# Kernel tuning notes

Hardware: AMD Instinct MI355X
Metric: run time of the kernel (lower is better)

## Reference

```python
import jax, jax.numpy as jnp
import numpy as np
from jax import lax


def _lstm_dir(x, W_ih, W_hh, b, reverse):
    # x: [B, T, D]; torch gate order i, f, g, o
    B, T, D = x.shape
    Hh = W_hh.shape[1]
    h0 = jnp.zeros((B, Hh), x.dtype)
    c0 = jnp.zeros((B, Hh), x.dtype)

    def step(carry, xt):
        h, c = carry
        g = xt @ W_ih.T + h @ W_hh.T + b
        i, f, gg, o = jnp.split(g, 4, axis=-1)
        c = jax.nn.sigmoid(f) * c + jax.nn.sigmoid(i) * jnp.tanh(gg)
        h = jax.nn.sigmoid(o) * jnp.tanh(c)
        return (h, c), h

    _, hs = lax.scan(step, (h0, c0), jnp.swapaxes(x, 0, 1), reverse=reverse)
    return jnp.swapaxes(hs, 0, 1)  # [B, T, Hh]


def _bilstm(x, w_ih_f, w_hh_f, b_f, w_ih_b, w_hh_b, b_b):
    fwd = _lstm_dir(x, w_ih_f, w_hh_f, b_f, reverse=False)
    bwd = _lstm_dir(x, w_ih_b, w_hh_b, b_b, reverse=True)
    return jnp.concatenate([fwd, bwd], axis=-1)


def setup_inputs() -> dict:
    key = jax.random.key(0)
    B, NS, L, H, LH, C = 8, 32, 128, 768, 256, 4
    ks = jax.random.split(key, 16)
    s = 0.05
    inp = {
        "hidden_states": jax.random.normal(ks[0], (B, NS, L, H), jnp.float32),
        "attention_mask": jax.random.randint(ks[1], (B, NS, L), 0, 2, jnp.int32),
        "wl_ih_f": jax.random.normal(ks[2], (4 * LH, H), jnp.float32) * s,
        "wl_hh_f": jax.random.normal(ks[3], (4 * LH, LH), jnp.float32) * s,
        "wl_b_f": jnp.zeros((4 * LH,), jnp.float32).at[LH:2 * LH].set(1.0),
        "wl_ih_b": jax.random.normal(ks[4], (4 * LH, H), jnp.float32) * s,
        "wl_hh_b": jax.random.normal(ks[5], (4 * LH, LH), jnp.float32) * s,
        "wl_b_b": jnp.zeros((4 * LH,), jnp.float32).at[LH:2 * LH].set(1.0),
        "ws_ih_f": jax.random.normal(ks[6], (4 * LH, 2 * LH), jnp.float32) * s,
        "ws_hh_f": jax.random.normal(ks[7], (4 * LH, LH), jnp.float32) * s,
        "ws_b_f": jnp.zeros((4 * LH,), jnp.float32).at[LH:2 * LH].set(1.0),
        "ws_ih_b": jax.random.normal(ks[8], (4 * LH, 2 * LH), jnp.float32) * s,
        "ws_hh_b": jax.random.normal(ks[9], (4 * LH, LH), jnp.float32) * s,
        "ws_b_b": jnp.zeros((4 * LH,), jnp.float32).at[LH:2 * LH].set(1.0),
        "cls_w": jax.random.uniform(ks[10], (C, 2 * LH), jnp.float32, -0.1, 0.1),
        "cls_b": jax.random.uniform(ks[11], (C,), jnp.float32, -0.1, 0.1),
    }
    return inp


def reference(hidden_states, attention_mask,
              wl_ih_f, wl_hh_f, wl_b_f, wl_ih_b, wl_hh_b, wl_b_b,
              ws_ih_f, ws_hh_f, ws_b_f, ws_ih_b, ws_hh_b, ws_b_b,
              cls_w, cls_b):
    B, NS, L, H = hidden_states.shape
    x = hidden_states.reshape(B * NS, L, H)
    m = attention_mask.reshape(B * NS, L).astype(x.dtype)

    # word-level bidirectional LSTM over each sentence
    h = _bilstm(x, wl_ih_f, wl_hh_f, wl_b_f, wl_ih_b, wl_hh_b, wl_b_b)  # [BN, L, 2LH]

    # per-sentence masked mean pooling (zeros for fully-masked sentences)
    cnt = m.sum(-1, keepdims=True)                    # [BN, 1]
    emb = jnp.einsum('btd,bt->bd', h, m) / jnp.maximum(cnt, 1.0)
    emb = jnp.where(cnt > 0, emb, 0.0)                # [BN, 2LH]
    emb = emb.reshape(B, NS, -1)

    # sentence-level bidirectional LSTM
    s = _bilstm(emb, ws_ih_f, ws_hh_f, ws_b_f, ws_ih_b, ws_hh_b, ws_b_b)  # [B, NS, 2LH]

    final = s[:, -1, :]  # dropout is identity in deterministic reference
    logits = final @ cls_w.T + cls_b
    return logits
```

## Files before the change

kernel.cpp:

```cpp
#include <hip/hip_runtime.h>
#include <math.h>


typedef __bf16 bf16x8 __attribute__((ext_vector_type(8)));
typedef float  f32x4  __attribute__((ext_vector_type(4)));

__device__ __forceinline__ float sigmoidf_(float x){ return 1.0f/(1.0f+expf(-x)); }
__device__ __forceinline__ unsigned short f2bf(float x){
    unsigned int b = __float_as_uint(x);
    b += 0x7FFFu + ((b>>16)&1u);
    return (unsigned short)(b>>16);
}
__device__ __forceinline__ float bf2f(unsigned short h){
    return __uint_as_float(((unsigned int)h)<<16);
}
__device__ __forceinline__ void split_bf(float x, unsigned short &hi, unsigned short &lo){
    hi = f2bf(x);
    lo = f2bf(x - bf2f(hi));
}
__device__ __forceinline__ uint4 pack8(const unsigned short* s){
    uint4 u;
    u.x = (unsigned)s[0] | ((unsigned)s[1]<<16);
    u.y = (unsigned)s[2] | ((unsigned)s[3]<<16);
    u.z = (unsigned)s[4] | ((unsigned)s[5]<<16);
    u.w = (unsigned)s[6] | ((unsigned)s[7]<<16);
    return u;
}

__device__ __forceinline__ void group_barrier(int* p, int members, int tid) {
    __syncthreads();
    if (tid == 0) {
        __hip_atomic_fetch_add(p, 1, __ATOMIC_RELAXED, __HIP_MEMORY_SCOPE_AGENT);
        int it = 0;
        while (__hip_atomic_load(p, __ATOMIC_RELAXED, __HIP_MEMORY_SCOPE_AGENT) < members) {
            __builtin_amdgcn_s_sleep(1);
            if (++it > (1<<22)) break;
        }
    }
    __builtin_amdgcn_fence(__ATOMIC_ACQUIRE, "workgroup");
    __syncthreads();
}

__device__ __forceinline__ unsigned tpat(int bid, int tid, int r) {
    unsigned v = (unsigned)bid * 1315423911u ^ (unsigned)tid * 2654435761u ^ 0x9E3779B9u;
    return r ? ~v : v;
}

__global__ void zero_f4(float4* __restrict__ p, int n) {
    int i = blockIdx.x * 256 + threadIdx.x;
    if (i < n) p[i] = make_float4(0.f, 0.f, 0.f, 0.f);
}

__global__ void prep_x(const float* __restrict__ X, unsigned short* __restrict__ Xsw) {
    int idx = blockIdx.x * 256 + threadIdx.x;
    int gblk = idx >> 6, ln = idx & 63;
    int mt = gblk / 24, kb = gblk - mt * 24;
    int m = mt * 16 + (ln & 15);
    int k = kb * 32 + (ln >> 4) * 8;
    const float* xp = X + (size_t)m * 768 + k;
    unsigned short hi[8], lo[8];
#pragma unroll
    for (int e = 0; e < 8; e += 4) {
        float4 v = *(const float4*)(xp + e);
        split_bf(v.x, hi[e+0], lo[e+0]);
        split_bf(v.y, hi[e+1], lo[e+1]);
        split_bf(v.z, hi[e+2], lo[e+2]);
        split_bf(v.w, hi[e+3], lo[e+3]);
    }
    *(uint4*)&Xsw[(size_t)gblk*1024 + ln*8]       = pack8(hi);
    *(uint4*)&Xsw[(size_t)gblk*1024 + 512 + ln*8] = pack8(lo);
}

__global__ void prep_wih_sw(const float* __restrict__ Wf, const float* __restrict__ Wb,
                            unsigned short* __restrict__ Wsw) {
    int idx = blockIdx.x * 256 + threadIdx.x;
    int gblk = idx >> 6, ln = idx & 63;
    int dir = gblk / 1536;
    int rem = gblk - dir * 1536;
    int ntile = rem / 24, kb = rem - ntile * 24;
    int j = ntile * 16 + (ln & 15);
    int k = kb * 32 + (ln >> 4) * 8;
    const float* wp = (dir ? Wb : Wf) + (size_t)j * 768 + k;
    unsigned short hi[8], lo[8];
#pragma unroll
    for (int e = 0; e < 8; e += 4) {
        float4 v = *(const float4*)(wp + e);
        split_bf(v.x, hi[e+0], lo[e+0]);
        split_bf(v.y, hi[e+1], lo[e+1]);
        split_bf(v.z, hi[e+2], lo[e+2]);
        split_bf(v.w, hi[e+3], lo[e+3]);
    }
    *(uint4*)&Wsw[(size_t)gblk*1024 + ln*8]       = pack8(hi);
    *(uint4*)&Wsw[(size_t)gblk*1024 + 512 + ln*8] = pack8(lo);
}

__global__ void prep_whh(const float* __restrict__ Wf, const float* __restrict__ Wb,
                         unsigned short* __restrict__ Wimg) {
    int idx = blockIdx.x * 256 + threadIdx.x;
    if (idx >= 524288) return;
    int dir = idx >> 18;
    int r   = idx & 262143;
    int u0t = r >> 14;
    int g   = (r >> 12) & 3;
    int u   = (r >> 8) & 15;
    int k   = r & 255;
    const float* W = dir ? Wb : Wf;
    float v = W[(size_t)(g*256 + u0t*16 + u) * 256 + k];
    unsigned short hi, lo; split_bf(v, hi, lo);
    size_t base = (size_t)(dir*16 + u0t) * 34816;
    Wimg[base + (g*16 + u)*264 + k]         = hi;
    Wimg[base + 16896 + (g*16 + u)*264 + k] = lo;
}

__global__ void transpose_whh(const float* __restrict__ Wf, const float* __restrict__ Wb,
                              float* __restrict__ Wt) {
    int idx = blockIdx.x * 256 + threadIdx.x;
    if (idx >= 524288) return;
    int dir = idx >> 18;
    int rem = idx & 262143;
    int k = rem >> 10;
    int j = rem & 1023;
    const float* Wp = dir ? Wb : Wf;
    Wt[idx] = Wp[j * 256 + k];
}

__global__ __launch_bounds__(256, 2) void proj_mfma(
    const unsigned short* __restrict__ Xsw,
    const unsigned short* __restrict__ Wihsw,
    const float* __restrict__ bfw, const float* __restrict__ bbw,
    float* __restrict__ Of, float* __restrict__ Ob)
{
    __shared__ unsigned short lds[24576];
    const int tid = threadIdx.x;
    const int nt = blockIdx.x;
    const int mt = blockIdx.y;
    const int sel = nt >> 3;
    const int ntl = nt & 7;
    const float* bias = sel ? bbw : bfw;
    float* Op = sel ? Ob : Of;
    const int wv = tid >> 6, ln = tid & 63;
    const int c = ln & 15, q = ln >> 4;

    f32x4 acc[4][8];
#pragma unroll
    for (int i = 0; i < 4; i++)
#pragma unroll
        for (int j = 0; j < 8; j++) acc[i][j] = f32x4{0.f,0.f,0.f,0.f};

    const unsigned short* Abase = Xsw + (size_t)(mt*16) * 24 * 1024;
    const unsigned short* Bbase = Wihsw + (size_t)(sel*64 + ntl*8) * 24 * 1024;

#pragma unroll 1
    for (int kb = 0; kb < 24; kb++) {
        __syncthreads();
#pragma unroll
        for (int jj = 0; jj < 12; jj++) {
            int cc = wv + 4*jj;
            int isB = (cc >= 32);
            int blk = isB ? ((cc - 32) >> 1) : (cc >> 1);
            int half = cc & 1;
            const unsigned short* src = (isB ? Bbase : Abase)
                                        + (size_t)(blk*24 + kb)*1024 + half*512 + ln*8;
            unsigned short* dst = lds + (isB ? 16384 : 0) + blk*1024 + half*512 + ln*8;
            __builtin_amdgcn_global_load_lds(
                (const __attribute__((address_space(1))) unsigned int*)src,
                (__attribute__((address_space(3))) unsigned int*)dst, 16, 0, 0);
        }
        __syncthreads();

        bf16x8 bhv[8], blv[8];
#pragma unroll
        for (int cb = 0; cb < 8; cb++) {
            bhv[cb] = *(const bf16x8*)&lds[16384 + cb*1024 + ln*8];
            blv[cb] = *(const bf16x8*)&lds[16384 + cb*1024 + 512 + ln*8];
        }
#pragma unroll
        for (int rb = 0; rb < 4; rb++) {
            int it = wv*4 + rb;
            bf16x8 ah = *(const bf16x8*)&lds[it*1024 + ln*8];
            bf16x8 al = *(const bf16x8*)&lds[it*1024 + 512 + ln*8];
#pragma unroll
            for (int cb = 0; cb < 8; cb++) {
                acc[rb][cb] = __builtin_amdgcn_mfma_f32_16x16x32_bf16(ah, bhv[cb], acc[rb][cb], 0,0,0);
                acc[rb][cb] = __builtin_amdgcn_mfma_f32_16x16x32_bf16(ah, blv[cb], acc[rb][cb], 0,0,0);
                acc[rb][cb] = __builtin_amdgcn_mfma_f32_16x16x32_bf16(al, bhv[cb], acc[rb][cb], 0,0,0);
            }
        }
    }

#pragma unroll
    for (int rb = 0; rb < 4; rb++) {
        int mbase = mt*256 + (wv*4 + rb)*16 + q*4;
#pragma unroll
        for (int cb = 0; cb < 8; cb++) {
            int j = ntl*128 + cb*16 + c;
            float bv = bias[j];
#pragma unroll
            for (int reg = 0; reg < 4; reg++) {
                int m = mbase + reg;
                int tt = m & 127, nn = m >> 7;
                Op[(size_t)(tt*256 + nn)*1024 + j] = acc[rb][cb][reg] + bv;
            }
        }
    }
}

__global__ __launch_bounds__(256, 1) void word_recur(
    const float* __restrict__ Gf, const float* __restrict__ Gb,
    const unsigned short* __restrict__ Wimg,
    unsigned short* __restrict__ hA, unsigned short* __restrict__ hB,
    const int* __restrict__ mask,
    float* __restrict__ pooled, int* __restrict__ cnt,
    int* __restrict__ pf, unsigned int* __restrict__ tstg)
{
    extern __shared__ char ldsbuf[];
    unsigned short* Hl = (unsigned short*)ldsbuf;
    float* gex   = (float*)(ldsbuf + 36864);
    int*   mk_lds= (int*)(ldsbuf + 46080);

    const int tid = threadIdx.x;
    const int bid = blockIdx.x;
    const int dir = (bid >> 3) & 1;
    const int nt  = bid & 7;
    const int u0t = bid >> 4;
    const int grp = bid & 15;
    const float* G = dir ? Gb : Gf;

    const int wv = tid >> 6, ln = tid & 63;
    const int c = ln & 15, q = ln >> 4;

    int* mycnt = cnt + grp * 136;

    bool fast;
    {
        unsigned* tl  = (unsigned*)ldsbuf;
        int* oks = (int*)(ldsbuf + 4096);
        int okl = 1;
#pragma unroll 1
        for (int r = 0; r < 2; r++) {
            __hip_atomic_store(&tstg[bid*256 + tid], tpat(bid, tid, r),
                               __ATOMIC_RELAXED, __HIP_MEMORY_SCOPE_AGENT);
            group_barrier(mycnt + 127 + 2*r, 16, tid);
            {
                int pbid = grp + 16*((u0t + 1 + wv) & 15);
                __builtin_amdgcn_global_load_lds(
                    (const __attribute__((address_space(1))) unsigned int*)
                        ((const char*)(tstg + pbid*256) + ln*16),
                    (__attribute__((address_space(3))) unsigned int*)(ldsbuf + wv*1024),
                    16, 0, 0x11 );
            }
            __syncthreads();
#pragma unroll
            for (int w2 = 0; w2 < 4; w2++) {
                int pb2 = grp + 16*((u0t + 1 + w2) & 15);
                okl &= (tl[w2*256 + tid] == tpat(pb2, tid, r)) ? 1 : 0;
            }
            group_barrier(mycnt + 128 + 2*r, 16, tid);
        }
        oks[tid] = okl;
        __syncthreads();
        if (tid == 0) {
            int o = 1;
            for (int i = 0; i < 256; i++) o &= oks[i];
            __hip_atomic_store(&pf[bid], o, __ATOMIC_RELAXED, __HIP_MEMORY_SCOPE_AGENT);
        }
        group_barrier(mycnt + 131, 16, tid);
        int f = 1;
#pragma unroll 1
        for (int k = 0; k < 16; k++)
            f &= __hip_atomic_load(&pf[grp + 16*k],
                                   __ATOMIC_RELAXED, __HIP_MEMORY_SCOPE_AGENT);
        fast = (f != 0);
    }

    {
        const char* msrc = (const char*)(mask + nt*32*128);
#pragma unroll
        for (int j = 0; j < 4; j++) {
            int i = wv + 4*j;
            __builtin_amdgcn_global_load_lds(
                (const __attribute__((address_space(1))) unsigned int*)(msrc + i*1024 + ln*16),
                (__attribute__((address_space(3))) unsigned int*)(((char*)mk_lds) + i*1024), 16, 0, 0);
        }
    }
    const unsigned short* wbase = Wimg + (size_t)(dir*16 + u0t) * 34816;
    bf16x8 wh_[8], wlo[8];
#pragma unroll
    for (int kb = 0; kb < 8; kb++) {
        wh_[kb] = *(const bf16x8*)&wbase[(wv*16 + c)*264 + kb*32 + q*8];
        wlo[kb] = *(const bf16x8*)&wbase[16896 + (wv*16 + c)*264 + kb*32 + q*8];
    }

    const int nl  = tid >> 3;
    const int up  = tid & 7;
    const int u0  = up*2;
    const int ug0 = u0t*16 + u0;
    const int n   = nt*32 + nl;

    float c0 = 0.f, c1 = 0.f, p0 = 0.f, p1 = 0.f;

    float2 gp[4];
    {
        const int te0 = dir ? 127 : 0;
        const float* Ga = G + (size_t)(te0*256 + n)*1024 + ug0;
#pragma unroll
        for (int g = 0; g < 4; g++) gp[g] = *(const float2*)&Ga[g*256];
    }

#pragma unroll 1
    for (int t = 0; t < 128; ++t) {
        const int te = dir ? (127 - t) : t;
        const unsigned short* hin = (t & 1) ? hB : hA;
        unsigned short* hout = ((t & 1) ? hA : hB) + (size_t)(dir*8 + nt) * 18432;

        if (fast) {
            const char* hsrc = (const char*)(hin + (size_t)(dir*8 + nt) * 18432);
#pragma unroll
            for (int j = 0; j < 9; j++) {
                int i = wv + 4*j;
                __builtin_amdgcn_global_load_lds(
                    (const __attribute__((address_space(1))) unsigned int*)(hsrc + i*1024 + ln*16),
                    (__attribute__((address_space(3))) unsigned int*)(ldsbuf + i*1024),
                    16, 0, 0x11 );
            }
        } else {
            const unsigned long long* hsrc =
                (const unsigned long long*)(hin + (size_t)(dir*8 + nt) * 18432);
            unsigned long long* hdst = (unsigned long long*)ldsbuf;
#pragma unroll
            for (int j = 0; j < 18; j++) {
                unsigned long long v = __hip_atomic_load(hsrc + tid + 256*j,
                        __ATOMIC_RELAXED, __HIP_MEMORY_SCOPE_AGENT);
                hdst[tid + 256*j] = v;
            }
        }
        __syncthreads();

        f32x4 acc[2];
        acc[0] = f32x4{0.f,0.f,0.f,0.f};
        acc[1] = f32x4{0.f,0.f,0.f,0.f};
#pragma unroll
        for (int kb = 0; kb < 8; kb++) {
#pragma unroll
            for (int sb = 0; sb < 2; sb++) {
                bf16x8 bh = *(const bf16x8*)&Hl[(sb*16 + c)*264 + kb*32 + q*8];
                bf16x8 bl = *(const bf16x8*)&Hl[8448 + (sb*16 + c)*264 + kb*32 + q*8];
                acc[sb] = __builtin_amdgcn_mfma_f32_16x16x32_bf16(wh_[kb], bh, acc[sb], 0, 0, 0);
                acc[sb] = __builtin_amdgcn_mfma_f32_16x16x32_bf16(wh_[kb], bl, acc[sb], 0, 0, 0);
                acc[sb] = __builtin_amdgcn_mfma_f32_16x16x32_bf16(wlo[kb], bh, acc[sb], 0, 0, 0);
            }
        }
#pragma unroll
        for (int sb = 0; sb < 2; sb++)
#pragma unroll
            for (int reg = 0; reg < 4; reg++)
                gex[(wv*16 + q*4 + reg)*36 + sb*16 + c] = acc[sb][reg];
        __syncthreads();

        float2 gpn[4];
        if (t < 127) {
            const int te1 = dir ? (126 - t) : (t + 1);
            const float* Ga = G + (size_t)(te1*256 + n)*1024 + ug0;
#pragma unroll
            for (int g = 0; g < 4; g++) gpn[g] = *(const float2*)&Ga[g*256];
        }

        const int mk = mk_lds[nl*128 + te];
        float iv0 = gex[(0*16 + u0)*36 + nl] + gp[0].x;
        float fv0 = gex[(1*16 + u0)*36 + nl] + gp[1].x;
        float gv0 = gex[(2*16 + u0)*36 + nl] + gp[2].x;
        float ov0 = gex[(3*16 + u0)*36 + nl] + gp[3].x;
        float iv1 = gex[(0*16 + u0+1)*36 + nl] + gp[0].y;
        float fv1 = gex[(1*16 + u0+1)*36 + nl] + gp[1].y;
        float gv1 = gex[(2*16 + u0+1)*36 + nl] + gp[2].y;
        float ov1 = gex[(3*16 + u0+1)*36 + nl] + gp[3].y;
        float cn0 = sigmoidf_(fv0)*c0 + sigmoidf_(iv0)*tanhf(gv0);
        float hn0 = sigmoidf_(ov0)*tanhf(cn0);
        float cn1 = sigmoidf_(fv1)*c1 + sigmoidf_(iv1)*tanhf(gv1);
        float hn1 = sigmoidf_(ov1)*tanhf(cn1);
        c0 = cn0; c1 = cn1;
        if (mk) { p0 += hn0; p1 += hn1; }
        if (t != 127) {
            unsigned short h0h, h0l, h1h, h1l;
            split_bf(hn0, h0h, h0l);
            split_bf(hn1, h1h, h1l);
            unsigned int dhi = (unsigned)h0h | ((unsigned)h1h << 16);
            unsigned int dlo = (unsigned)h0l | ((unsigned)h1l << 16);
            unsigned int* hw = (unsigned int*)hout;
            __hip_atomic_store(&hw[nl*132 + u0t*8 + up], dhi,
                               __ATOMIC_RELAXED, __HIP_MEMORY_SCOPE_AGENT);
            __hip_atomic_store(&hw[4224 + nl*132 + u0t*8 + up], dlo,
                               __ATOMIC_RELAXED, __HIP_MEMORY_SCOPE_AGENT);
        }

        if (t < 127) {
            group_barrier(mycnt + t, 16, tid);
#pragma unroll
            for (int g = 0; g < 4; g++) gp[g] = gpn[g];
        }
    }

    *(float2*)&pooled[n*512 + dir*256 + ug0] = make_float2(p0, p1);
}

__global__ __launch_bounds__(256) void word_step_mfma(
    const float* __restrict__ Gf, const float* __restrict__ Gb,
    const unsigned short* __restrict__ Wimg,
    const unsigned short* __restrict__ hin_img,
    unsigned short* __restrict__ hout_img,
    const int* __restrict__ mask,
    float* __restrict__ c_st, float* __restrict__ pooled, int t)
{
    extern __shared__ char ldsbuf[];
    unsigned short* Wl = (unsigned short*)ldsbuf;
    unsigned short* Hl = Wl + 34816;
    float* gex = (float*)(ldsbuf + 69632 + 36864);

    const int tid = threadIdx.x;
    const int bid = blockIdx.x;
    const int dir = bid >> 7;
    const int u0t = (bid >> 3) & 15;
    const int nt  = bid & 7;
    const int te  = dir ? (127 - t) : t;
    const float* G = dir ? Gb : Gf;

    const int wv = tid >> 6, ln = tid & 63;
    const int c = ln & 15, q = ln >> 4;

    {
        const char* wsrc = (const char*)(Wimg + (size_t)(dir*16 + u0t) * 34816);
        const char* hsrc = (const char*)(hin_img + (size_t)(dir*8 + nt) * 18432);
        char* wdst = (char*)Wl;
        char* hdst = (char*)Hl;
#pragma unroll
        for (int j = 0; j < 17; j++) {
            int i = wv + 4*j;
            __builtin_amdgcn_global_load_lds(
                (const __attribute__((address_space(1))) unsigned int*)(wsrc + i*1024 + ln*16),
                (__attribute__((address_space(3))) unsigned int*)(wdst + i*1024), 16, 0, 0);
        }
#pragma unroll
        for (int j = 0; j < 9; j++) {
            int i = wv + 4*j;
            __builtin_amdgcn_global_load_lds(
                (const __attribute__((address_space(1))) unsigned int*)(hsrc + i*1024 + ln*16),
                (__attribute__((address_space(3))) unsigned int*)(hdst + i*1024), 16, 0, 0);
        }
    }

    const int uu = tid & 15;
    const int np = tid >> 4;
    const int uglob = u0t*16 + uu;
    const int n_a = nt*32 + np*2;
    float gpre[8]; int mk0, mk1; float cold0, cold1, pold0, pold1;
    {
        const float* Ga = G + (size_t)(te*256 + n_a)*1024 + uglob;
        const float* Gc = Ga + 1024;
#pragma unroll
        for (int g = 0; g < 4; g++) { gpre[g] = Ga[g*256]; gpre[4+g] = Gc[g*256]; }
        mk0 = mask[n_a*128 + te];
        mk1 = mask[(n_a + 1)*128 + te];
        cold0 = c_st[dir*65536 + n_a*256 + uglob];
        cold1 = c_st[dir*65536 + (n_a + 1)*256 + uglob];
        pold0 = pooled[n_a*512 + dir*256 + uglob];
        pold1 = pooled[(n_a + 1)*512 + dir*256 + uglob];
    }
    __syncthreads();

    f32x4 acc[2];
    acc[0] = f32x4{0.f,0.f,0.f,0.f};
    acc[1] = f32x4{0.f,0.f,0.f,0.f};
#pragma unroll
    for (int kb = 0; kb < 8; kb++) {
        bf16x8 ahh = *(const bf16x8*)&Wl[(wv*16 + c)*264 + kb*32 + q*8];
        bf16x8 all_ = *(const bf16x8*)&Wl[16896 + (wv*16 + c)*264 + kb*32 + q*8];
#pragma unroll
        for (int sb = 0; sb < 2; sb++) {
            bf16x8 bh = *(const bf16x8*)&Hl[(sb*16 + c)*264 + kb*32 + q*8];
            bf16x8 bl = *(const bf16x8*)&Hl[8448 + (sb*16 + c)*264 + kb*32 + q*8];
            acc[sb] = __builtin_amdgcn_mfma_f32_16x16x32_bf16(ahh, bh, acc[sb], 0, 0, 0);
            acc[sb] = __builtin_amdgcn_mfma_f32_16x16x32_bf16(ahh, bl, acc[sb], 0, 0, 0);
            acc[sb] = __builtin_amdgcn_mfma_f32_16x16x32_bf16(all_, bh, acc[sb], 0, 0, 0);
        }
    }
#pragma unroll
    for (int sb = 0; sb < 2; sb++)
#pragma unroll
        for (int reg = 0; reg < 4; reg++)
            gex[(wv*16 + q*4 + reg)*36 + sb*16 + c] = acc[sb][reg];
    __syncthreads();

    unsigned short* hout = hout_img + (size_t)(dir*8 + nt) * 18432;
    {
        int nl = np*2;
        float iv = gex[(0*16 + uu)*36 + nl] + gpre[0];
        float fv = gex[(1*16 + uu)*36 + nl] + gpre[1];
        float gv = gex[(2*16 + uu)*36 + nl] + gpre[2];
        float ov = gex[(3*16 + uu)*36 + nl] + gpre[3];
        float cn = sigmoidf_(fv)*cold0 + sigmoidf_(iv)*tanhf(gv);
        float hn = sigmoidf_(ov)*tanhf(cn);
        c_st[dir*65536 + n_a*256 + uglob] = cn;
        unsigned short hh, hl; split_bf(hn, hh, hl);
        hout[nl*264 + uglob] = hh;
        hout[8448 + nl*264 + uglob] = hl;
        if (mk0) pooled[n_a*512 + dir*256 + uglob] = pold0 + hn;
    }
    {
        int nl = np*2 + 1;
        float iv = gex[(0*16 + uu)*36 + nl] + gpre[4];
        float fv = gex[(1*16 + uu)*36 + nl] + gpre[5];
        float gv = gex[(2*16 + uu)*36 + nl] + gpre[6];
        float ov = gex[(3*16 + uu)*36 + nl] + gpre[7];
        float cn = sigmoidf_(fv)*cold1 + sigmoidf_(iv)*tanhf(gv);
        float hn = sigmoidf_(ov)*tanhf(cn);
        c_st[dir*65536 + (n_a+1)*256 + uglob] = cn;
        unsigned short hh, hl; split_bf(hn, hh, hl);
        hout[nl*264 + uglob] = hh;
        hout[8448 + nl*264 + uglob] = hl;
        if (mk1) pooled[(n_a+1)*512 + dir*256 + uglob] = pold1 + hn;
    }
}

__global__ __launch_bounds__(256) void gemm_proj(
    const float* __restrict__ A, int M, int K,
    const float* __restrict__ Wf, const float* __restrict__ Wb,
    const float* __restrict__ bf, const float* __restrict__ bb,
    float* __restrict__ Of, float* __restrict__ Ob)
{
    __shared__ float As[16][132];
    __shared__ float Bs[16][132];
    const int t = threadIdx.x;
    const int n0 = blockIdx.x * 128;
    const int m0 = blockIdx.y * 128;
    const int sel = (n0 >= 1024);
    const float* Wp = sel ? Wb : Wf;
    const float* bp = sel ? bb : bf;
    float* Op = sel ? Ob : Of;
    const int n0d = n0 & 1023;
    const int tm = t >> 4;
    const int tn = t & 15;

    float acc[8][8];
#pragma unroll
    for (int i = 0; i < 8; i++)
#pragma unroll
        for (int j = 0; j < 8; j++) acc[i][j] = 0.f;

    for (int k0 = 0; k0 < K; k0 += 16) {
        __syncthreads();
#pragma unroll
        for (int rr = 0; rr < 2; rr++) {
            int idx = t + rr * 256;
            int row = idx >> 2, kq = idx & 3;
            float4 v = *(const float4*)&A[(size_t)(m0 + row) * K + k0 + kq * 4];
            As[kq*4+0][row] = v.x; As[kq*4+1][row] = v.y;
            As[kq*4+2][row] = v.z; As[kq*4+3][row] = v.w;
        }
#pragma unroll
        for (int rr = 0; rr < 2; rr++) {
            int idx = t + rr * 256;
            int row = idx >> 2, kq = idx & 3;
            float4 v = *(const float4*)&Wp[(size_t)(n0d + row) * K + k0 + kq * 4];
            Bs[kq*4+0][row] = v.x; Bs[kq*4+1][row] = v.y;
            Bs[kq*4+2][row] = v.z; Bs[kq*4+3][row] = v.w;
        }
        __syncthreads();
#pragma unroll
        for (int k = 0; k < 16; k++) {
            float4 a0 = *(const float4*)&As[k][tm*4];
            float4 a1 = *(const float4*)&As[k][tm*4+64];
            float4 b0 = *(const float4*)&Bs[k][tn*4];
            float4 b1 = *(const float4*)&Bs[k][tn*4+64];
            float av[8] = {a0.x,a0.y,a0.z,a0.w,a1.x,a1.y,a1.z,a1.w};
            float bv[8] = {b0.x,b0.y,b0.z,b0.w,b1.x,b1.y,b1.z,b1.w};
#pragma unroll
            for (int i = 0; i < 8; i++)
#pragma unroll
                for (int j = 0; j < 8; j++)
                    acc[i][j] += av[i] * bv[j];
        }
    }

#pragma unroll
    for (int ih = 0; ih < 2; ih++) {
#pragma unroll
        for (int i = 0; i < 4; i++) {
            int m = m0 + ih*64 + tm*4 + i;
#pragma unroll
            for (int jh = 0; jh < 2; jh++) {
                int col = n0d + jh*64 + tn*4;
                float4 bias4 = *(const float4*)&bp[col];
                float4 r;
                r.x = acc[ih*4+i][jh*4+0] + bias4.x;
                r.y = acc[ih*4+i][jh*4+1] + bias4.y;
                r.z = acc[ih*4+i][jh*4+2] + bias4.z;
                r.w = acc[ih*4+i][jh*4+3] + bias4.w;
                *(float4*)&Op[(size_t)m * 1024 + col] = r;
            }
        }
    }
}

__global__ __launch_bounds__(256) void pool_div(float* __restrict__ pooled,
                                                const int* __restrict__ mask) {
    __shared__ float red[256];
    int n = blockIdx.x, t = threadIdx.x;
    red[t] = (t < 128) ? (float)mask[n*128 + t] : 0.f;
    __syncthreads();
    for (int off = 128; off > 0; off >>= 1) {
        if (t < off) red[t] += red[t + off];
        __syncthreads();
    }
    float inv = 1.0f / fmaxf(red[0], 1.0f);
    pooled[n*512 + t] *= inv;
    pooled[n*512 + 256 + t] *= inv;
}

__global__ __launch_bounds__(256) void sent_recur(
    const float* __restrict__ Gsf, const float* __restrict__ Gsb,
    const float* __restrict__ Whf, const float* __restrict__ Whb,
    float* __restrict__ hs0, float* __restrict__ hs1,
    float* __restrict__ final_h, int* __restrict__ cnt,
    int* __restrict__ pf, unsigned int* __restrict__ tstg)
{
    extern __shared__ char sbuf[];
    float* Wlds  = (float*)sbuf;
    float* h_lds = Wlds + 128*260;
    float* part  = h_lds + 256;
    float* ex    = part + 256;

    const int tid = threadIdx.x;
    const int bid = blockIdx.x;
    const int dir = (bid >> 3) & 1;
    const int b   = bid & 7;
    const int ut  = bid >> 4;
    const int grp = bid & 15;
    const float* Gs = dir ? Gsb : Gsf;
    const float* Wh = dir ? Whb : Whf;
    const int wv = tid >> 6, ln = tid & 63;

    int* mycnt = cnt + grp * 40;

    bool fast;
    {
        unsigned* tl  = (unsigned*)sbuf;
        int* oks = (int*)(sbuf + 4096);
        int okl = 1;
#pragma unroll 1
        for (int r = 0; r < 2; r++) {
            __hip_atomic_store(&tstg[bid*256 + tid], tpat(bid, tid, r) ^ 0x5A5A5A5Au,
                               __ATOMIC_RELAXED, __HIP_MEMORY_SCOPE_AGENT);
            group_barrier(mycnt + 31 + 2*r, 8, tid);
            {
                int pbid = grp + 16*((ut + 1 + wv) & 7);
                __builtin_amdgcn_global_load_lds(
                    (const __attribute__((address_space(1))) unsigned int*)
                        ((const char*)(tstg + pbid*256) + ln*16),
                    (__attribute__((address_space(3))) unsigned int*)(sbuf + wv*1024),
                    16, 0, 0x11 );
            }
            __syncthreads();
#pragma unroll
            for (int w2 = 0; w2 < 4; w2++) {
                int pb2 = grp + 16*((ut + 1 + w2) & 7);
                okl &= (tl[w2*256 + tid] == (tpat(pb2, tid, r) ^ 0x5A5A5A5Au)) ? 1 : 0;
            }
            group_barrier(mycnt + 32 + 2*r, 8, tid);
        }
        oks[tid] = okl;
        __syncthreads();
        if (tid == 0) {
            int o = 1;
            for (int i = 0; i < 256; i++) o &= oks[i];
            __hip_atomic_store(&pf[bid], o, __ATOMIC_RELAXED, __HIP_MEMORY_SCOPE_AGENT);
        }
        group_barrier(mycnt + 35, 8, tid);
        int f = 1;
#pragma unroll 1
        for (int k = 0; k < 8; k++)
            f &= __hip_atomic_load(&pf[grp + 16*k],
                                   __ATOMIC_RELAXED, __HIP_MEMORY_SCOPE_AGENT);
        fast = (f != 0);
    }

#pragma unroll
    for (int j = 0; j < 32; j++) {
        int chunk = wv + 4*j;
        int g = chunk >> 5, u2 = chunk & 31;
        const char* src = (const char*)(Wh + (size_t)(g*256 + ut*32 + u2) * 256);
        __builtin_amdgcn_global_load_lds(
            (const __attribute__((address_space(1))) unsigned int*)(src + ln*16),
            (__attribute__((address_space(3))) unsigned int*)((char*)(Wlds + chunk*260)), 16, 0, 0);
    }

    const int jloc = tid & 127, kh = tid >> 7;
    float creg = 0.f;

#pragma unroll 1
    for (int s = 0; s < 32; ++s) {
        const int t_eff = dir ? (31 - s) : s;
        const float* hin = (s & 1) ? hs1 : hs0;
        float* hout = (s & 1) ? hs0 : hs1;

        if (fast) {
            if (wv == 0)
                __builtin_amdgcn_global_load_lds(
                    (const __attribute__((address_space(1))) unsigned int*)
                        ((const char*)(hin + dir*2048 + b*256) + ln*16),
                    (__attribute__((address_space(3))) unsigned int*)((char*)h_lds),
                    16, 0, 0x11 );
        } else if (tid < 128) {
            const unsigned long long* hp =
                (const unsigned long long*)(hin + dir*2048 + b*256);
            unsigned long long v = __hip_atomic_load(hp + tid,
                    __ATOMIC_RELAXED, __HIP_MEMORY_SCOPE_AGENT);
            *(unsigned long long*)&h_lds[tid*2] = v;
        }

        float gsv = 0.f;
        if (tid < 128)
            gsv = Gs[(size_t)(b*32 + t_eff)*1024 + (jloc >> 5)*256 + ut*32 + (jloc & 31)];

        __syncthreads();

        const float* wrow = Wlds + jloc*260 + kh*128;
        const float* hrow = h_lds + kh*128;
        float acc = 0.f;
#pragma unroll
        for (int kc = 0; kc < 32; kc++) {
            float4 w4 = *(const float4*)(wrow + kc*4);
            float4 h4 = *(const float4*)(hrow + kc*4);
            acc += w4.x*h4.x + w4.y*h4.y + w4.z*h4.z + w4.w*h4.w;
        }
        part[tid] = acc;
        __syncthreads();
        if (tid < 128)
            ex[(jloc >> 5)*33 + (jloc & 31)] = part[tid] + part[tid + 128] + gsv;
        __syncthreads();
        if (tid < 32) {
            float iv = ex[0*33 + tid];
            float fv = ex[1*33 + tid];
            float gv = ex[2*33 + tid];
            float ov = ex[3*33 + tid];
            float cn = sigmoidf_(fv)*creg + sigmoidf_(iv)*tanhf(gv);
            float hn = sigmoidf_(ov)*tanhf(cn);
            creg = cn;
            int u = ut*32 + tid;
            __hip_atomic_store((unsigned int*)&hout[dir*2048 + b*256 + u],
                               __float_as_uint(hn),
                               __ATOMIC_RELAXED, __HIP_MEMORY_SCOPE_AGENT);
            if (t_eff == 31) final_h[b*512 + dir*256 + u] = hn;
        }
        if (s < 31) group_barrier(mycnt + s, 8, tid);
    }
}

__global__ __launch_bounds__(256) void sent_step(
    const float* __restrict__ Gsf, const float* __restrict__ Gsb,
    const float* __restrict__ Wt,
    const float* __restrict__ h_in, float* __restrict__ h_out,
    float* __restrict__ c_s, float* __restrict__ final_h, int s)
{
    __shared__ float h_lds[256];
    __shared__ float part[256];
    __shared__ float ex[4][33];
    const int tid = threadIdx.x;
    const int bx = blockIdx.x;
    const int dir = bx >> 6;
    const int rb = bx & 63;
    const int b = rb >> 3;
    const int ut = rb & 7;
    const int u0 = ut * 32;
    const int t_eff = dir ? (31 - s) : s;
    const float* Gs = dir ? Gsb : Gsf;

    if (tid < 64) {
        float4 v = *(const float4*)&h_in[dir*2048 + b*256 + tid*4];
        *(float4*)&h_lds[tid*4] = v;
    }
    __syncthreads();

    const int kh = tid >> 7;
    const int rr = tid & 127;
    const int g = rr >> 5;
    const int uu = rr & 31;
    const int j = g*256 + u0 + uu;
    const float* wp = Wt + dir*262144 + kh*128*1024 + j;
    float acc = 0.f;
#pragma unroll 8
    for (int k = 0; k < 128; k++)
        acc += wp[k*1024] * h_lds[kh*128 + k];
    part[tid] = acc;
    __syncthreads();
    if (tid < 128) ex[g][uu] = part[tid] + part[tid + 128];
    __syncthreads();

    if (tid < 32) {
        int u = u0 + tid;
        size_t gb = (size_t)(b*32 + t_eff)*1024 + u;
        float iv = ex[0][tid] + Gs[gb];
        float fv = ex[1][tid] + Gs[gb + 256];
        float gv = ex[2][tid] + Gs[gb + 512];
        float ov = ex[3][tid] + Gs[gb + 768];
        int ci = dir*2048 + b*256 + u;
        float cold = c_s[ci];
        float cn = sigmoidf_(fv)*cold + sigmoidf_(iv)*tanhf(gv);
        float hn = sigmoidf_(ov)*tanhf(cn);
        c_s[ci] = cn;
        h_out[ci] = hn;
        if (t_eff == 31) final_h[b*512 + dir*256 + u] = hn;
    }
}

__global__ __launch_bounds__(256) void logits_k(const float* __restrict__ fh,
                                                const float* __restrict__ cw,
                                                const float* __restrict__ cb,
                                                float* __restrict__ out) {
    __shared__ float red[256];
    int tid = threadIdx.x;
    int o = tid >> 3;
    int b = o >> 2; int c = o & 3;
    int pp = tid & 7;
    float acc = 0.f;
    const float* fv = fh + b*512 + pp*64;
    const float* wv = cw + c*512 + pp*64;
#pragma unroll 8
    for (int e = 0; e < 64; e++) acc += fv[e]*wv[e];
    red[tid] = acc;
    __syncthreads();
    if (pp == 0) {
        float s = 0.f;
#pragma unroll
        for (int qq = 0; qq < 8; qq++) s += red[o*8 + qq];
        out[o] = s + cb[c];
    }
}

extern "C" void kernel_launch(void* const* d_in, const int* in_sizes, int n_in,
                              void* d_out, int out_size, void* d_ws, size_t ws_size,
                              hipStream_t stream) {
    const float* X       = (const float*)d_in[0];
    const int*   mask    = (const int*)d_in[1];
    const float* wl_ih_f = (const float*)d_in[2];
    const float* wl_hh_f = (const float*)d_in[3];
    const float* wl_b_f  = (const float*)d_in[4];
    const float* wl_ih_b = (const float*)d_in[5];
    const float* wl_hh_b = (const float*)d_in[6];
    const float* wl_b_b  = (const float*)d_in[7];
    const float* ws_ih_f = (const float*)d_in[8];
    const float* ws_hh_f = (const float*)d_in[9];
    const float* ws_b_f  = (const float*)d_in[10];
    const float* ws_ih_b = (const float*)d_in[11];
    const float* ws_hh_b = (const float*)d_in[12];
    const float* ws_b_b  = (const float*)d_in[13];
    const float* cls_w   = (const float*)d_in[14];
    const float* cls_b   = (const float*)d_in[15];
    float* out = (float*)d_out;
    float* w = (float*)d_ws;
    (void)in_sizes; (void)n_in; (void)out_size; (void)ws_size;

    float* Gf     = w;
    float* Gb     = Gf + 33554432;
    float* Gsf    = Gb + 33554432;
    float* Gsb    = Gsf + 262144;
    float* Wt     = Gsb + 262144;
    int*   cnt_w  = (int*)Wt;
    int*   cnt_s  = cnt_w + 2176;
    int*   pf     = cnt_s + 640;
    unsigned int* tstg = (unsigned int*)(pf + 256);
    float* finalh = Wt + 524288;
    float* pooled = finalh + 4096;
    float* c_st   = pooled + 131072;
    float* hs0    = c_st + 131072;
    float* hs1    = hs0 + 4096;
    float* cs     = hs1 + 4096;
    unsigned short* hA = (unsigned short*)(cs + 4096);
    unsigned short* hB = hA + 294912;
    unsigned short* Xsw   = hB + 294912;
    unsigned short* Wihsw = Xsw + 50331648;
    unsigned short* Wimg  = Wihsw + 3145728;

    zero_f4<<<412, 256, 0, stream>>>((float4*)pooled, 105472);
    zero_f4<<<3, 256, 0, stream>>>((float4*)cnt_w, 704);
    prep_x<<<12288, 256, 0, stream>>>(X, Xsw);
    prep_wih_sw<<<768, 256, 0, stream>>>(wl_ih_f, wl_ih_b, Wihsw);
    prep_whh<<<2048, 256, 0, stream>>>(wl_hh_f, wl_hh_b, Wimg);

    proj_mfma<<<dim3(16, 128), 256, 0, stream>>>(Xsw, Wihsw, wl_b_f, wl_b_b, Gf, Gb);

    {
        const float* gfp = Gf; const float* gbp = Gb;
        const unsigned short* wimg = Wimg;
        unsigned short* ha = hA; unsigned short* hb = hB;
        const int* mk = mask;
        float* pl = pooled; int* cw = cnt_w; int* pfp = pf; unsigned int* tp = tstg;
        void* args[] = { &gfp, &gbp, &wimg, &ha, &hb, &mk, &pl, &cw, &pfp, &tp };
        hipError_t e = hipLaunchCooperativeKernel((const void*)word_recur,
                           dim3(256), dim3(256), args, 62464, stream);
        if (e != hipSuccess) {
            hipFuncSetAttribute((const void*)word_step_mfma,
                                hipFuncAttributeMaxDynamicSharedMemorySize, 115712);
            for (int t = 0; t < 128; t++) {
                const unsigned short* hin = (t & 1) ? hB : hA;
                unsigned short* hout      = (t & 1) ? hA : hB;
                word_step_mfma<<<256, 256, 115712, stream>>>(Gf, Gb, Wimg, hin, hout,
                                                             mask, c_st, pooled, t);
            }
        }
    }

    pool_div<<<256, 256, 0, stream>>>(pooled, mask);

    gemm_proj<<<dim3(16, 2), 256, 0, stream>>>(pooled, 256, 512,
                                               ws_ih_f, ws_ih_b, ws_b_f, ws_b_b,
                                               Gsf, Gsb);

    {
        hipFuncSetAttribute((const void*)sent_recur,
                            hipFuncAttributeMaxDynamicSharedMemorySize, 135696);
        const float* gsf = Gsf; const float* gsb = Gsb;
        const float* whf = ws_hh_f; const float* whb = ws_hh_b;
        float* h0 = hs0; float* h1 = hs1;
        float* fh = finalh; int* cse = cnt_s; int* pfp = pf; unsigned int* tp = tstg;
        void* args[] = { &gsf, &gsb, &whf, &whb, &h0, &h1, &fh, &cse, &pfp, &tp };
        hipError_t e = hipLaunchCooperativeKernel((const void*)sent_recur,
                           dim3(128), dim3(256), args, 135696, stream);
        if (e != hipSuccess) {
            transpose_whh<<<2048, 256, 0, stream>>>(ws_hh_f, ws_hh_b, Wt);
            for (int s = 0; s < 32; s++) {
                float* hin  = (s & 1) ? hs1 : hs0;
                float* hout = (s & 1) ? hs0 : hs1;
                sent_step<<<128, 256, 0, stream>>>(Gsf, Gsb, Wt, hin, hout, cs, finalh, s);
            }
        }
    }

    logits_k<<<1, 256, 0, stream>>>(finalh, cls_w, cls_b, out);
}
```

Measured before the change: 1.010 ms.

## Replace counter barriers with per-member epoch flags, drop cooperative launch, fuse pooling divide

Both persistent recurrence kernels now sync each timestep through an epoch-flag barrier. Every member block stores its current step into its own padded slot, and up to 16 threads poll the slots in parallel, instead of all blocks atomically incrementing one shared per-step counter. The cooperative launches become ordinary launches, which avoids cooperative-launch overhead but relies on all blocks being co-resident without a guarantee. The masked-mean divide is folded into the word kernel's final store, removing the separate pool_div launch on the fast path.

```diff
diff --git a/kernel.cpp b/kernel.cpp
--- a/kernel.cpp
+++ b/kernel.cpp
@@ -33,6 +33,24 @@
         __hip_atomic_fetch_add(p, 1, __ATOMIC_RELAXED, __HIP_MEMORY_SCOPE_AGENT);
         int it = 0;
         while (__hip_atomic_load(p, __ATOMIC_RELAXED, __HIP_MEMORY_SCOPE_AGENT) < members) {
+            __builtin_amdgcn_s_sleep(1);
+            if (++it > (1<<22)) break;
+        }
+    }
+    __builtin_amdgcn_fence(__ATOMIC_ACQUIRE, "workgroup");
+    __syncthreads();
+}
+
+__device__ __forceinline__ void epoch_barrier(int* base, int member, int members,
+                                              int epoch, int tid) {
+    __syncthreads();
+    if (tid == 0)
+        __hip_atomic_store(base + member*16, epoch,
+                           __ATOMIC_RELAXED, __HIP_MEMORY_SCOPE_AGENT);
+    if (tid < members) {
+        int it = 0;
+        while (__hip_atomic_load(base + tid*16,
+                   __ATOMIC_RELAXED, __HIP_MEMORY_SCOPE_AGENT) < epoch) {
             __builtin_amdgcn_s_sleep(1);
             if (++it > (1<<22)) break;
         }
@@ -210,7 +228,7 @@
     const unsigned short* __restrict__ Wimg,
     unsigned short* __restrict__ hA, unsigned short* __restrict__ hB,
     const int* __restrict__ mask,
-    float* __restrict__ pooled, int* __restrict__ cnt,
+    float* __restrict__ pooled, int* __restrict__ cnt, int* __restrict__ eflag,
     int* __restrict__ pf, unsigned int* __restrict__ tstg)
 {
     extern __shared__ char ldsbuf[];
@@ -229,7 +247,8 @@
     const int wv = tid >> 6, ln = tid & 63;
     const int c = ln & 15, q = ln >> 4;
 
-    int* mycnt = cnt + grp * 136;
+    int* mycnt = cnt + grp * 8;
+    int* myflag = eflag + grp * 256;
 
     bool fast;
     {
@@ -240,7 +259,7 @@
         for (int r = 0; r < 2; r++) {
             __hip_atomic_store(&tstg[bid*256 + tid], tpat(bid, tid, r),
                                __ATOMIC_RELAXED, __HIP_MEMORY_SCOPE_AGENT);
-            group_barrier(mycnt + 127 + 2*r, 16, tid);
+            group_barrier(mycnt + 2*r, 16, tid);
             {
                 int pbid = grp + 16*((u0t + 1 + wv) & 15);
                 __builtin_amdgcn_global_load_lds(
@@ -255,7 +274,7 @@
                 int pb2 = grp + 16*((u0t + 1 + w2) & 15);
                 okl &= (tl[w2*256 + tid] == tpat(pb2, tid, r)) ? 1 : 0;
             }
-            group_barrier(mycnt + 128 + 2*r, 16, tid);
+            group_barrier(mycnt + 1 + 2*r, 16, tid);
         }
         oks[tid] = okl;
         __syncthreads();
@@ -264,7 +283,7 @@
             for (int i = 0; i < 256; i++) o &= oks[i];
             __hip_atomic_store(&pf[bid], o, __ATOMIC_RELAXED, __HIP_MEMORY_SCOPE_AGENT);
         }
-        group_barrier(mycnt + 131, 16, tid);
+        group_barrier(mycnt + 4, 16, tid);
         int f = 1;
 #pragma unroll 1
         for (int k = 0; k < 16; k++)
@@ -394,13 +413,17 @@
         }
 
         if (t < 127) {
-            group_barrier(mycnt + t, 16, tid);
+            epoch_barrier(myflag, u0t, 16, t + 1, tid);
 #pragma unroll
             for (int g = 0; g < 4; g++) gp[g] = gpn[g];
         }
     }
 
-    *(float2*)&pooled[n*512 + dir*256 + ug0] = make_float2(p0, p1);
+    int cntN = 0;
+#pragma unroll 1
+    for (int te2 = 0; te2 < 128; ++te2) cntN += mk_lds[nl*128 + te2];
+    float inv = 1.0f / fmaxf((float)cntN, 1.0f);
+    *(float2*)&pooled[n*512 + dir*256 + ug0] = make_float2(p0*inv, p1*inv);
 }
 
 __global__ __launch_bounds__(256) void word_step_mfma(
@@ -620,7 +643,7 @@
     const float* __restrict__ Gsf, const float* __restrict__ Gsb,
     const float* __restrict__ Whf, const float* __restrict__ Whb,
     float* __restrict__ hs0, float* __restrict__ hs1,
-    float* __restrict__ final_h, int* __restrict__ cnt,
+    float* __restrict__ final_h, int* __restrict__ cnt, int* __restrict__ eflag,
     int* __restrict__ pf, unsigned int* __restrict__ tstg)
 {
     extern __shared__ char sbuf[];
@@ -639,7 +662,8 @@
     const float* Wh = dir ? Whb : Whf;
     const int wv = tid >> 6, ln = tid & 63;
 
-    int* mycnt = cnt + grp * 40;
+    int* mycnt = cnt + grp * 8;
+    int* myflag = eflag + grp * 128;
 
     bool fast;
     {
@@ -650,7 +674,7 @@
         for (int r = 0; r < 2; r++) {
             __hip_atomic_store(&tstg[bid*256 + tid], tpat(bid, tid, r) ^ 0x5A5A5A5Au,
                                __ATOMIC_RELAXED, __HIP_MEMORY_SCOPE_AGENT);
-            group_barrier(mycnt + 31 + 2*r, 8, tid);
+            group_barrier(mycnt + 2*r, 8, tid);
             {
                 int pbid = grp + 16*((ut + 1 + wv) & 7);
                 __builtin_amdgcn_global_load_lds(
@@ -665,7 +689,7 @@
                 int pb2 = grp + 16*((ut + 1 + w2) & 7);
                 okl &= (tl[w2*256 + tid] == (tpat(pb2, tid, r) ^ 0x5A5A5A5Au)) ? 1 : 0;
             }
-            group_barrier(mycnt + 32 + 2*r, 8, tid);
+            group_barrier(mycnt + 1 + 2*r, 8, tid);
         }
         oks[tid] = okl;
         __syncthreads();
@@ -674,7 +698,7 @@
             for (int i = 0; i < 256; i++) o &= oks[i];
             __hip_atomic_store(&pf[bid], o, __ATOMIC_RELAXED, __HIP_MEMORY_SCOPE_AGENT);
         }
-        group_barrier(mycnt + 35, 8, tid);
+        group_barrier(mycnt + 4, 8, tid);
         int f = 1;
 #pragma unroll 1
         for (int k = 0; k < 8; k++)
@@ -751,7 +775,7 @@
                                __ATOMIC_RELAXED, __HIP_MEMORY_SCOPE_AGENT);
             if (t_eff == 31) final_h[b*512 + dir*256 + u] = hn;
         }
-        if (s < 31) group_barrier(mycnt + s, 8, tid);
+        if (s < 31) epoch_barrier(myflag, ut, 8, s + 1, tid);
     }
 }
 
@@ -865,8 +889,10 @@
     float* Gsb    = Gsf + 262144;
     float* Wt     = Gsb + 262144;
     int*   cnt_w  = (int*)Wt;
-    int*   cnt_s  = cnt_w + 2176;
-    int*   pf     = cnt_s + 640;
+    int*   cnt_s  = cnt_w + 128;
+    int*   eflag_w= cnt_s + 128;
+    int*   eflag_s= eflag_w + 4096;
+    int*   pf     = eflag_s + 2048;
     unsigned int* tstg = (unsigned int*)(pf + 256);
     float* finalh = Wt + 524288;
     float* pooled = finalh + 4096;
@@ -881,7 +907,7 @@
     unsigned short* Wimg  = Wihsw + 3145728;
 
     zero_f4<<<412, 256, 0, stream>>>((float4*)pooled, 105472);
-    zero_f4<<<3, 256, 0, stream>>>((float4*)cnt_w, 704);
+    zero_f4<<<7, 256, 0, stream>>>((float4*)cnt_w, 1600);
     prep_x<<<12288, 256, 0, stream>>>(X, Xsw);
     prep_wih_sw<<<768, 256, 0, stream>>>(wl_ih_f, wl_ih_b, Wihsw);
     prep_whh<<<2048, 256, 0, stream>>>(wl_hh_f, wl_hh_b, Wimg);
@@ -889,14 +915,10 @@
     proj_mfma<<<dim3(16, 128), 256, 0, stream>>>(Xsw, Wihsw, wl_b_f, wl_b_b, Gf, Gb);
 
     {
-        const float* gfp = Gf; const float* gbp = Gb;
-        const unsigned short* wimg = Wimg;
-        unsigned short* ha = hA; unsigned short* hb = hB;
-        const int* mk = mask;
-        float* pl = pooled; int* cw = cnt_w; int* pfp = pf; unsigned int* tp = tstg;
-        void* args[] = { &gfp, &gbp, &wimg, &ha, &hb, &mk, &pl, &cw, &pfp, &tp };
-        hipError_t e = hipLaunchCooperativeKernel((const void*)word_recur,
-                           dim3(256), dim3(256), args, 62464, stream);
+        (void)hipGetLastError();
+        word_recur<<<256, 256, 62464, stream>>>(Gf, Gb, Wimg, hA, hB, mask,
+                                                pooled, cnt_w, eflag_w, pf, tstg);
+        hipError_t e = hipGetLastError();
         if (e != hipSuccess) {
             hipFuncSetAttribute((const void*)word_step_mfma,
                                 hipFuncAttributeMaxDynamicSharedMemorySize, 115712);
@@ -906,10 +928,9 @@
                 word_step_mfma<<<256, 256, 115712, stream>>>(Gf, Gb, Wimg, hin, hout,
                                                              mask, c_st, pooled, t);
             }
-        }
-    }
-
-    pool_div<<<256, 256, 0, stream>>>(pooled, mask);
+            pool_div<<<256, 256, 0, stream>>>(pooled, mask);
+        }
+    }
 
     gemm_proj<<<dim3(16, 2), 256, 0, stream>>>(pooled, 256, 512,
                                                ws_ih_f, ws_ih_b, ws_b_f, ws_b_b,
@@ -918,13 +939,11 @@
     {
         hipFuncSetAttribute((const void*)sent_recur,
                             hipFuncAttributeMaxDynamicSharedMemorySize, 135696);
-        const float* gsf = Gsf; const float* gsb = Gsb;
-        const float* whf = ws_hh_f; const float* whb = ws_hh_b;
-        float* h0 = hs0; float* h1 = hs1;
-        float* fh = finalh; int* cse = cnt_s; int* pfp = pf; unsigned int* tp = tstg;
-        void* args[] = { &gsf, &gsb, &whf, &whb, &h0, &h1, &fh, &cse, &pfp, &tp };
-        hipError_t e = hipLaunchCooperativeKernel((const void*)sent_recur,
-                           dim3(128), dim3(256), args, 135696, stream);
+        (void)hipGetLastError();
+        sent_recur<<<128, 256, 135696, stream>>>(Gsf, Gsb, ws_hh_f, ws_hh_b,
+                                                 hs0, hs1, finalh, cnt_s, eflag_s,
+                                                 pf, tstg);
+        hipError_t e = hipGetLastError();
         if (e != hipSuccess) {
             transpose_whh<<<2048, 256, 0, stream>>>(ws_hh_f, ws_hh_b, Wt);
             for (int s = 0; s < 32; s++) {
```

Measured after the change: 1.014 ms. No clear change (+0.4%).
